# Kernel tuning notes

Hardware: AMD Instinct MI355X
Metric: run time of the kernel (lower is better)

## Reference

```python
import math
import jax, jax.numpy as jnp
import numpy as np

B, C, H, W = 8, 512, 32, 32
NUM_HEADS = 8
HEAD_DIM = C // NUM_HEADS


def setup_inputs() -> dict:
    key = jax.random.key(0)
    ks = jax.random.split(key, 5)
    scale = 1.0 / math.sqrt(C)
    return {
        "x": jax.random.normal(ks[0], (B, C, H, W), dtype=jnp.float32),
        "Wq": jax.random.normal(ks[1], (C, C), dtype=jnp.float32) * scale,
        "bq": jnp.zeros((C,), dtype=jnp.float32),
        "Wk": jax.random.normal(ks[2], (C, C), dtype=jnp.float32) * scale,
        "bk": jnp.zeros((C,), dtype=jnp.float32),
        "Wv": jax.random.normal(ks[3], (C, C), dtype=jnp.float32) * scale,
        "bv": jnp.zeros((C,), dtype=jnp.float32),
        "Wo": jax.random.normal(ks[4], (C, C), dtype=jnp.float32) * scale,
        "bo": jnp.zeros((C,), dtype=jnp.float32),
    }


def reference(x, Wq, bq, Wk, bk, Wv, bv, Wo, bo):
    b, c, h, w = x.shape
    t = h * w
    # (B,C,H,W) -> (B,T,C) token sequence
    xt = x.reshape(b, c, t).transpose(0, 2, 1)
    Q = xt @ Wq + bq
    K = xt @ Wk + bk
    V = xt @ Wv + bv
    # (B,T,C) -> (B,nh,T,hd)
    def split_heads(z):
        return z.reshape(b, t, NUM_HEADS, HEAD_DIM).transpose(0, 2, 1, 3)
    Qh, Kh, Vh = split_heads(Q), split_heads(K), split_heads(V)
    S = jnp.einsum("bhqd,bhkd->bhqk", Qh, Kh) / math.sqrt(HEAD_DIM)
    A = jax.nn.softmax(S, axis=-1)  # dropout p=0.0 -> identity
    Y = jnp.einsum("bhqk,bhkd->bhqd", A, Vh)
    Y = Y.transpose(0, 2, 1, 3).reshape(b, t, c)
    O = Y @ Wo + bo
    out = xt + O
    return out.transpose(0, 2, 1).reshape(b, c, h, w)
```

## Files before the change

kernel.cpp:

```cpp
#include <hip/hip_runtime.h>
#include <hip/hip_bf16.h>

#define B_  8
#define C_  512
#define T_  1024
#define NH_ 8
#define HD_ 64

#define QSCALE 0.1803368801111243f

using short8 = __attribute__((ext_vector_type(8))) short;
using f32x4  = __attribute__((ext_vector_type(4))) float;
using f32x16 = __attribute__((ext_vector_type(16))) float;
using us4    = __attribute__((ext_vector_type(4))) unsigned short;

__device__ __forceinline__ unsigned short f2bf(float f) {
    unsigned u = __builtin_bit_cast(unsigned, f);
    u += 0x7fff + ((u >> 16) & 1);
    return (unsigned short)(u >> 16);
}
__device__ __forceinline__ unsigned pack2bf(float lo, float hi) {
    __hip_bfloat162 h = __float22bfloat162_rn(float2{lo, hi});
    unsigned u;
    __builtin_memcpy(&u, &h, 4);
    return u;
}

__device__ __forceinline__ void gload_lds16(const ushort* g, ushort* l) {
    __builtin_amdgcn_global_load_lds(
        (const __attribute__((address_space(1))) void*)g,
        (__attribute__((address_space(3))) void*)l, 16, 0, 0);
}

__global__ __launch_bounds__(256) void k_transpose_x(const float* __restrict__ x,
                                                     ushort* __restrict__ xt) {
    __shared__ float tile[32][33];
    int b = blockIdx.z, t0 = blockIdx.x * 32, c0 = blockIdx.y * 32;
    int tx = threadIdx.x & 31, ty = threadIdx.x >> 5;
#pragma unroll
    for (int i = 0; i < 4; i++)
        tile[ty + i * 8][tx] = x[((size_t)b * C_ + c0 + ty + i * 8) * T_ + t0 + tx];
    __syncthreads();
#pragma unroll
    for (int i = 0; i < 4; i++)
        xt[((size_t)b * T_ + t0 + ty + i * 8) * C_ + c0 + tx] = f2bf(tile[tx][ty + i * 8]);
}

__global__ __launch_bounds__(256) void k_transpose_w(const float* __restrict__ Wq,
                                                     const float* __restrict__ Wk,
                                                     const float* __restrict__ Wv,
                                                     const float* __restrict__ Wo,
                                                     ushort* __restrict__ Wqkvt,
                                                     ushort* __restrict__ Wot) {
    __shared__ float tile[32][33];
    int m = blockIdx.z;
    const float* W = (m == 0) ? Wq : (m == 1) ? Wk : (m == 2) ? Wv : Wo;
    ushort* dst = (m < 3) ? (Wqkvt + (size_t)m * C_ * C_) : Wot;
    float scale = (m == 0) ? QSCALE : 1.0f;
    int k0 = blockIdx.x * 32, n0 = blockIdx.y * 32;
    int tx = threadIdx.x & 31, ty = threadIdx.x >> 5;
#pragma unroll
    for (int i = 0; i < 4; i++)
        tile[ty + i * 8][tx] = W[(size_t)(k0 + ty + i * 8) * C_ + n0 + tx];
    __syncthreads();
#pragma unroll
    for (int i = 0; i < 4; i++)
        dst[(size_t)(n0 + ty + i * 8) * C_ + k0 + tx] = f2bf(tile[tx][ty + i * 8] * scale);
}

__device__ __forceinline__ void gemm_core(const ushort* __restrict__ A,
                                          const ushort* __restrict__ Bt,
                                          int row0, int col0, int tid,
                                          ushort (*As)[8192], ushort (*Bs)[8192],
                                          f32x4 acc[4][4]) {
    f32x4 zero = {0.f, 0.f, 0.f, 0.f};
#pragma unroll
    for (int i = 0; i < 4; i++)
#pragma unroll
        for (int j = 0; j < 4; j++) acc[i][j] = zero;
    int lane = tid & 63, w = tid >> 6;
    int ql = lane & 15, g = lane >> 4;
    int wm = (w >> 1) * 64, wn = (w & 1) * 64;
    int srow = lane >> 3;
    int scol8 = (lane & 7) ^ (srow & 7);

#pragma unroll
    for (int i = 0; i < 4; i++) {
        int c = w * 4 + i;
        int r = c * 8 + srow;
        gload_lds16(A + (size_t)(row0 + r) * C_ + scol8 * 8, As[0] + c * 512);
        gload_lds16(Bt + (size_t)(col0 + r) * C_ + scol8 * 8, Bs[0] + c * 512);
    }
    __syncthreads();

    for (int kt = 0; kt < 8; kt++) {
        int cur = kt & 1;
        if (kt < 7) {
            int k0 = (kt + 1) * 64;
#pragma unroll
            for (int i = 0; i < 4; i++) {
                int c = w * 4 + i;
                int r = c * 8 + srow;
                gload_lds16(A + (size_t)(row0 + r) * C_ + k0 + scol8 * 8, As[cur ^ 1] + c * 512);
                gload_lds16(Bt + (size_t)(col0 + r) * C_ + k0 + scol8 * 8, Bs[cur ^ 1] + c * 512);
            }
        }
        const ushort* Ac = As[cur];
        const ushort* Bc = Bs[cur];
        __builtin_amdgcn_s_setprio(1);
#pragma unroll
        for (int s = 0; s < 2; s++) {
            short8 a[4], b[4];
            int cs = ((4 * s + g) ^ (ql & 7)) * 8;
#pragma unroll
            for (int mt = 0; mt < 4; mt++)
                a[mt] = *(const short8*)(Ac + (wm + mt * 16 + ql) * 64 + cs);
#pragma unroll
            for (int nt = 0; nt < 4; nt++)
                b[nt] = *(const short8*)(Bc + (wn + nt * 16 + ql) * 64 + cs);
#pragma unroll
            for (int mt = 0; mt < 4; mt++)
#pragma unroll
                for (int nt = 0; nt < 4; nt++)
                    acc[mt][nt] = __builtin_amdgcn_mfma_f32_16x16x32_bf16(
                        a[mt], b[nt], acc[mt][nt], 0, 0, 0);
        }
        __builtin_amdgcn_s_setprio(0);
        __syncthreads();
    }
}

__global__ __launch_bounds__(256) void k_qkv(const ushort* __restrict__ xt,
                                             const ushort* __restrict__ Wqkvt,
                                             const float* __restrict__ bq,
                                             const float* __restrict__ bk,
                                             const float* __restrict__ bv,
                                             ushort* __restrict__ Qh,
                                             ushort* __restrict__ Kh,
                                             ushort* __restrict__ Vt) {
    __shared__ __align__(16) ushort As[2][8192];
    __shared__ __align__(16) ushort Bs[2][8192];
    f32x4 acc[4][4];
    int tid = threadIdx.x;
    int row0 = blockIdx.x * 128, col0 = blockIdx.y * 128;
    gemm_core(xt, Wqkvt, row0, col0, tid, As, Bs, acc);
    int lane = tid & 63, w = tid >> 6;
    int wm = (w >> 1) * 64, wn = (w & 1) * 64;
    int which = col0 >> 9;
    const float* bias = (which == 0) ? bq : (which == 1) ? bk : bv;
    float bscale = (which == 0) ? QSCALE : 1.0f;
#pragma unroll
    for (int mt = 0; mt < 4; mt++) {
        int grow0 = row0 + wm + mt * 16 + ((lane >> 4) << 2);
        int b = grow0 >> 10, t = grow0 & 1023;
#pragma unroll
        for (int nt = 0; nt < 4; nt++) {
            int gcol = col0 + wn + nt * 16 + (lane & 15);
            int hc = gcol & 511;
            float bsv = bias[hc] * bscale;
            int h = hc >> 6, d = hc & 63;
            if (which == 2) {
                us4 pk;
#pragma unroll
                for (int r = 0; r < 4; r++) pk[r] = f2bf(acc[mt][nt][r] + bsv);
                *(us4*)(Vt + ((size_t)(b * NH_ + h) * HD_ + d) * T_ + t) = pk;
            } else {
                ushort* dst = (which == 0) ? Qh : Kh;
#pragma unroll
                for (int r = 0; r < 4; r++)
                    dst[((size_t)(b * NH_ + h) * T_ + t + r) * HD_ + d] =
                        f2bf(acc[mt][nt][r] + bsv);
            }
        }
    }
}

__global__ __launch_bounds__(512) void k_attn(const ushort* __restrict__ Qh,
                                              const ushort* __restrict__ Kh,
                                              const ushort* __restrict__ Vt,
                                              ushort* __restrict__ Y) {
    __shared__ __align__(16) ushort Ks[2][64 * 64];
    __shared__ __align__(16) ushort Vs[2][64 * 64];
    int tid = threadIdx.x, lane = tid & 63, w = tid >> 6;
    int hi = lane >> 5, l31 = lane & 31, l7 = lane & 7;
    int bh = blockIdx.x & 63, q0 = (blockIdx.x >> 6) * 256;
    int b = bh >> 3, h = bh & 7;
    int srow = lane >> 3;
    int scol8 = l7 ^ (srow & 7);
    const ushort* Kbase = Kh + (size_t)bh * T_ * HD_;
    const ushort* Vbase = Vt + (size_t)bh * HD_ * T_;

    short8 qa[4];
#pragma unroll
    for (int s = 0; s < 4; s++)
        qa[s] = *(const short8*)(Qh + ((size_t)bh * T_ + q0 + w * 32 + l31) * HD_ +
                                 s * 16 + hi * 8);

    f32x16 o0, o1;
#pragma unroll
    for (int i = 0; i < 16; i++) { o0[i] = 0.f; o1[i] = 0.f; }
    float lsum = 0.f;

    {
        int r = w * 8 + srow;
        gload_lds16(Kbase + (size_t)r * HD_ + scol8 * 8, Ks[0] + w * 512);
        gload_lds16(Vbase + (size_t)r * T_ + scol8 * 8, Vs[0] + w * 512);
    }
    __syncthreads();

    for (int t = 0; t < 16; t++) {
        int cur = t & 1;
        const ushort* Kc = Ks[cur];
        const ushort* Vc = Vs[cur];
        if (t < 15) {
            int kv0 = (t + 1) * 64;
            int r = w * 8 + srow;
            gload_lds16(Kbase + (size_t)(kv0 + r) * HD_ + scol8 * 8, Ks[cur ^ 1] + w * 512);
            gload_lds16(Vbase + (size_t)r * T_ + kv0 + scol8 * 8, Vs[cur ^ 1] + w * 512);
        }

        f32x16 sT0, sT1;
#pragma unroll
        for (int i = 0; i < 16; i++) { sT0[i] = 0.f; sT1[i] = 0.f; }
        __builtin_amdgcn_s_setprio(1);
#pragma unroll
        for (int s = 0; s < 4; s++) {
            int cs = ((2 * s + hi) ^ l7) * 8;
            short8 ka0 = *(const short8*)(Kc + l31 * 64 + cs);
            short8 ka1 = *(const short8*)(Kc + (32 + l31) * 64 + cs);
            sT0 = __builtin_amdgcn_mfma_f32_32x32x16_bf16(ka0, qa[s], sT0, 0, 0, 0);
            sT1 = __builtin_amdgcn_mfma_f32_32x32x16_bf16(ka1, qa[s], sT1, 0, 0, 0);
        }
        __builtin_amdgcn_s_setprio(0);

        unsigned pkv0[8], pkv1[8];
        float ts = 0.f;
#pragma unroll
        for (int i = 0; i < 8; i++) {
            float a0 = __builtin_amdgcn_exp2f(sT0[2 * i]);
            float a1 = __builtin_amdgcn_exp2f(sT0[2 * i + 1]);
            float b0 = __builtin_amdgcn_exp2f(sT1[2 * i]);
            float b1 = __builtin_amdgcn_exp2f(sT1[2 * i + 1]);
            pkv0[i] = pack2bf(a0, a1);
            pkv1[i] = pack2bf(b0, b1);
            ts += (a0 + a1) + (b0 + b1);
        }
        lsum += ts;

        __builtin_amdgcn_s_setprio(1);
#pragma unroll
        for (int t4 = 0; t4 < 4; t4++) {
            const int h2 = t4 & 1;
            unsigned c0, c1, c2v, c3v;
            if (t4 < 2) {
                c0 = pkv0[4 * h2 + 0]; c2v = pkv0[4 * h2 + 2];
                c1 = pkv0[4 * h2 + 1]; c3v = pkv0[4 * h2 + 3];
            } else {
                c0 = pkv1[4 * h2 + 0]; c2v = pkv1[4 * h2 + 2];
                c1 = pkv1[4 * h2 + 1]; c3v = pkv1[4 * h2 + 3];
            }
            asm("v_permlane32_swap_b32 %0, %1" : "+v"(c0), "+v"(c2v));
            asm("v_permlane32_swap_b32 %0, %1" : "+v"(c1), "+v"(c3v));
            unsigned au[4] = {c0, c1, c2v, c3v};
            short8 pa;
            __builtin_memcpy(&pa, au, 16);
            int cs = ((2 * t4 + hi) ^ l7) * 8;
            short8 vb0 = *(const short8*)(Vc + l31 * 64 + cs);
            short8 vb1 = *(const short8*)(Vc + (32 + l31) * 64 + cs);
            o0 = __builtin_amdgcn_mfma_f32_32x32x16_bf16(pa, vb0, o0, 0, 0, 0);
            o1 = __builtin_amdgcn_mfma_f32_32x32x16_bf16(pa, vb1, o1, 0, 0, 0);
        }
        __builtin_amdgcn_s_setprio(0);
        __syncthreads();
    }

    float linv = 1.0f / (lsum + __shfl_xor(lsum, 32));
#pragma unroll
    for (int r = 0; r < 16; r++) {
        int qr = (r & 3) + 8 * (r >> 2) + 4 * hi;
        float li = __shfl(linv, qr);
        int trow = q0 + w * 32 + qr;
        size_t base = ((size_t)b * T_ + trow) * C_ + h * HD_;
        Y[base + l31] = f2bf(o0[r] * li);
        Y[base + 32 + l31] = f2bf(o1[r] * li);
    }
}

__global__ __launch_bounds__(256) void k_oproj(const ushort* __restrict__ Y,
                                               const ushort* __restrict__ Wot,
                                               const float* __restrict__ bo,
                                               const float* __restrict__ x,
                                               float* __restrict__ out) {
    __shared__ __align__(16) ushort As[2][8192];
    __shared__ __align__(16) ushort Bs[2][8192];
    f32x4 acc[4][4];
    int tid = threadIdx.x;
    int row0 = blockIdx.x * 128, col0 = blockIdx.y * 128;
    gemm_core(Y, Wot, row0, col0, tid, As, Bs, acc);
    int lane = tid & 63, w = tid >> 6;
    int wm = (w >> 1) * 64, wn = (w & 1) * 64;
#pragma unroll
    for (int mt = 0; mt < 4; mt++) {
        int grow0 = row0 + wm + mt * 16 + ((lane >> 4) << 2);
        int b = grow0 >> 10, t = grow0 & 1023;
#pragma unroll
        for (int nt = 0; nt < 4; nt++) {
            int c = col0 + wn + nt * 16 + (lane & 15);
            float bsv = bo[c];
            size_t off = ((size_t)b * C_ + c) * T_ + t;
            float4 xv = *(const float4*)(x + off);
            float4 ov;
            ov.x = acc[mt][nt][0] + xv.x + bsv;
            ov.y = acc[mt][nt][1] + xv.y + bsv;
            ov.z = acc[mt][nt][2] + xv.z + bsv;
            ov.w = acc[mt][nt][3] + xv.w + bsv;
            *(float4*)(out + off) = ov;
        }
    }
}

extern "C" void kernel_launch(void* const* d_in, const int* in_sizes, int n_in,
                              void* d_out, int out_size, void* d_ws, size_t ws_size,
                              hipStream_t stream) {
    const float* x  = (const float*)d_in[0];
    const float* Wq = (const float*)d_in[1];
    const float* bq = (const float*)d_in[2];
    const float* Wk = (const float*)d_in[3];
    const float* bk = (const float*)d_in[4];
    const float* Wv = (const float*)d_in[5];
    const float* bv = (const float*)d_in[6];
    const float* Wo = (const float*)d_in[7];
    const float* bo = (const float*)d_in[8];
    float* out = (float*)d_out;

    char* ws = (char*)d_ws;
    ushort* xt    = (ushort*)(ws + 0);
    ushort* Wqkvt = (ushort*)(ws + 8388608);
    ushort* Wot   = (ushort*)(ws + 9961472);
    ushort* Qh    = (ushort*)(ws + 10485760);
    ushort* Kh    = (ushort*)(ws + 18874368);
    ushort* Vt    = (ushort*)(ws + 27262976);
    ushort* Yw    = xt;

    k_transpose_x<<<dim3(32, 16, 8), 256, 0, stream>>>(x, xt);
    k_transpose_w<<<dim3(16, 16, 4), 256, 0, stream>>>(Wq, Wk, Wv, Wo, Wqkvt, Wot);
    k_qkv<<<dim3(64, 12), 256, 0, stream>>>(xt, Wqkvt, bq, bk, bv, Qh, Kh, Vt);
    k_attn<<<dim3(256), 512, 0, stream>>>(Qh, Kh, Vt, Yw);
    k_oproj<<<dim3(64, 4), 256, 0, stream>>>(Yw, Wot, bo, x, out);
}
```

Baseline: 80.78 us.

## Remap GEMM blocks per XCD and halve attention block size

The QKV and output-projection GEMMs now use a flattened 1D grid. Block indices are remapped so that consecutive blocks landing on the same XCD share row tiles, which should improve L2 reuse of the activation rows. The attention kernel drops from 512 threads covering 256 queries to 256 threads covering 128 queries, with each warp loading two K/V chunks, doubling the grid to 512 blocks. The smaller attention blocks spread work across more CUs but load each K/V tile twice as often overall.

```diff
diff --git a/kernel.cpp b/kernel.cpp
--- a/kernel.cpp
+++ b/kernel.cpp
@@ -142,7 +142,10 @@
     __shared__ __align__(16) ushort Bs[2][8192];
     f32x4 acc[4][4];
     int tid = threadIdx.x;
-    int row0 = blockIdx.x * 128, col0 = blockIdx.y * 128;
+    int L = blockIdx.x;
+    int n = L >> 3, xcd = L & 7;
+    int row0 = (xcd * 8 + (n & 7)) * 128;
+    int col0 = (n >> 3) * 128;
     gemm_core(xt, Wqkvt, row0, col0, tid, As, Bs, acc);
     int lane = tid & 63, w = tid >> 6;
     int wm = (w >> 1) * 64, wn = (w & 1) * 64;
@@ -175,7 +178,7 @@
     }
 }
 
-__global__ __launch_bounds__(512) void k_attn(const ushort* __restrict__ Qh,
+__global__ __launch_bounds__(256) void k_attn(const ushort* __restrict__ Qh,
                                               const ushort* __restrict__ Kh,
                                               const ushort* __restrict__ Vt,
                                               ushort* __restrict__ Y) {
@@ -183,7 +186,7 @@
     __shared__ __align__(16) ushort Vs[2][64 * 64];
     int tid = threadIdx.x, lane = tid & 63, w = tid >> 6;
     int hi = lane >> 5, l31 = lane & 31, l7 = lane & 7;
-    int bh = blockIdx.x & 63, q0 = (blockIdx.x >> 6) * 256;
+    int bh = blockIdx.x & 63, q0 = (blockIdx.x >> 6) * 128;
     int b = bh >> 3, h = bh & 7;
     int srow = lane >> 3;
     int scol8 = l7 ^ (srow & 7);
@@ -201,10 +204,12 @@
     for (int i = 0; i < 16; i++) { o0[i] = 0.f; o1[i] = 0.f; }
     float lsum = 0.f;
 
-    {
-        int r = w * 8 + srow;
-        gload_lds16(Kbase + (size_t)r * HD_ + scol8 * 8, Ks[0] + w * 512);
-        gload_lds16(Vbase + (size_t)r * T_ + scol8 * 8, Vs[0] + w * 512);
+#pragma unroll
+    for (int i = 0; i < 2; i++) {
+        int c = w * 2 + i;
+        int r = c * 8 + srow;
+        gload_lds16(Kbase + (size_t)r * HD_ + scol8 * 8, Ks[0] + c * 512);
+        gload_lds16(Vbase + (size_t)r * T_ + scol8 * 8, Vs[0] + c * 512);
     }
     __syncthreads();
 
@@ -214,9 +219,13 @@
         const ushort* Vc = Vs[cur];
         if (t < 15) {
             int kv0 = (t + 1) * 64;
-            int r = w * 8 + srow;
-            gload_lds16(Kbase + (size_t)(kv0 + r) * HD_ + scol8 * 8, Ks[cur ^ 1] + w * 512);
-            gload_lds16(Vbase + (size_t)r * T_ + kv0 + scol8 * 8, Vs[cur ^ 1] + w * 512);
+#pragma unroll
+            for (int i = 0; i < 2; i++) {
+                int c = w * 2 + i;
+                int r = c * 8 + srow;
+                gload_lds16(Kbase + (size_t)(kv0 + r) * HD_ + scol8 * 8, Ks[cur ^ 1] + c * 512);
+                gload_lds16(Vbase + (size_t)r * T_ + kv0 + scol8 * 8, Vs[cur ^ 1] + c * 512);
+            }
         }
 
         f32x16 sT0, sT1;
@@ -295,7 +304,10 @@
     __shared__ __align__(16) ushort Bs[2][8192];
     f32x4 acc[4][4];
     int tid = threadIdx.x;
-    int row0 = blockIdx.x * 128, col0 = blockIdx.y * 128;
+    int L = blockIdx.x;
+    int n = L >> 3, xcd = L & 7;
+    int row0 = (xcd * 8 + (n & 7)) * 128;
+    int col0 = (n >> 3) * 128;
     gemm_core(Y, Wot, row0, col0, tid, As, Bs, acc);
     int lane = tid & 63, w = tid >> 6;
     int wm = (w >> 1) * 64, wn = (w & 1) * 64;
@@ -344,7 +356,7 @@
 
     k_transpose_x<<<dim3(32, 16, 8), 256, 0, stream>>>(x, xt);
     k_transpose_w<<<dim3(16, 16, 4), 256, 0, stream>>>(Wq, Wk, Wv, Wo, Wqkvt, Wot);
-    k_qkv<<<dim3(64, 12), 256, 0, stream>>>(xt, Wqkvt, bq, bk, bv, Qh, Kh, Vt);
-    k_attn<<<dim3(256), 512, 0, stream>>>(Qh, Kh, Vt, Yw);
-    k_oproj<<<dim3(64, 4), 256, 0, stream>>>(Yw, Wot, bo, x, out);
-}
+    k_qkv<<<dim3(768), 256, 0, stream>>>(xt, Wqkvt, bq, bk, bv, Qh, Kh, Vt);
+    k_attn<<<dim3(512), 256, 0, stream>>>(Qh, Kh, Vt, Yw);
+    k_oproj<<<dim3(256), 256, 0, stream>>>(Yw, Wot, bo, x, out);
+}
```

Result: no change. 80.26 us (-0.6%).
